# Performance work log

Hardware: AMD Instinct MI355X
Metric: run time of the kernel (lower is better)

The kernel has to match this reference:

```python
import jax, jax.numpy as jnp
import numpy as np
import math

ATTN_TEMP = 1.0


def bilinear_sample(fea, gx, gy):
    """fea: [B,C,Hs,Ws]; gx, gy: [B,N] pixel coords (align_corners=True), zero padding."""
    B, C, Hs, Ws = fea.shape
    x0 = jnp.floor(gx)
    y0 = jnp.floor(gy)
    x1 = x0 + 1.0
    y1 = y0 + 1.0
    wx1 = gx - x0
    wx0 = 1.0 - wx1
    wy1 = gy - y0
    wy0 = 1.0 - wy1
    flat = fea.reshape(B, C, Hs * Ws)

    def gather(xi, yi, w):
        valid = (xi >= 0) & (xi <= Ws - 1) & (yi >= 0) & (yi <= Hs - 1)
        xi_c = jnp.clip(xi, 0, Ws - 1).astype(jnp.int32)
        yi_c = jnp.clip(yi, 0, Hs - 1).astype(jnp.int32)
        idx = yi_c * Ws + xi_c  # [B,N]
        vals = jnp.take_along_axis(flat, idx[:, None, :], axis=2)  # [B,C,N]
        return vals * (w * valid.astype(fea.dtype))[:, None, :]

    return (gather(x0, y0, wx0 * wy0) + gather(x1, y0, wx1 * wy0)
            + gather(x0, y1, wx0 * wy1) + gather(x1, y1, wx1 * wy1))


def homo_warp(src_fea, src_proj, ref_proj, depth_values):
    """Plane-sweep homography warp. src_fea [B,C,Hs,Ws], projs [B,4,4], depth [B,D,Hr,Wr]."""
    B, C, Hs, Ws = src_fea.shape
    _, D, Hr, Wr = depth_values.shape
    proj = src_proj @ jnp.linalg.inv(ref_proj)
    rot = proj[:, :3, :3]
    trans = proj[:, :3, 3]  # [B,3]
    y, x = jnp.meshgrid(jnp.arange(Hr, dtype=src_fea.dtype),
                        jnp.arange(Wr, dtype=src_fea.dtype), indexing='ij')
    ones = jnp.ones(Hr * Wr, dtype=src_fea.dtype)
    xyz = jnp.stack([x.ravel(), y.ravel(), ones])  # [3,N]
    rot_xyz = jnp.einsum('bij,jn->bin', rot, xyz)  # [B,3,N]
    # [B,3,D,N]
    proj_xyz = rot_xyz[:, :, None, :] * depth_values.reshape(B, 1, D, Hr * Wr) \
               + trans[:, :, None, None]
    z = proj_xyz[:, 2]
    z = jnp.where(z == 0, jnp.asarray(1e-9, z.dtype), z)
    px = (proj_xyz[:, 0] / z).reshape(B, -1)  # pixel coords (equivalent to normalize+align_corners)
    py = (proj_xyz[:, 1] / z).reshape(B, -1)
    warped = bilinear_sample(src_fea, px, py)  # [B,C,D*Hr*Wr]
    return warped.reshape(B, C, D, Hr, Wr)


def make_proj(p):
    """p: [B,2,4,4] (extrinsic, intrinsic) -> combined [B,4,4]."""
    top = jnp.einsum('bij,bjk->bik', p[:, 1, :3, :3], p[:, 0, :3, :4])
    return p[:, 0].at[:, :3, :4].set(top)


def setup_inputs() -> dict:
    key = jax.random.key(0)
    k1, k2, k3 = jax.random.split(key, 3)
    V, B, C, H, W, D, G = 5, 2, 32, 128, 128, 32, 8
    features = jax.random.normal(k1, (V, B, C, H, W), dtype=jnp.float32)
    rng = np.random.default_rng(0)
    ext = np.tile(np.eye(4, dtype=np.float32), (B, V, 1, 1))
    ext[..., :3, :3] += 0.01 * rng.normal(size=(B, V, 3, 3)).astype(np.float32)
    ext[..., :3, 3] += 0.1 * rng.normal(size=(B, V, 3)).astype(np.float32)
    intr = np.tile(np.eye(4, dtype=np.float32), (B, V, 1, 1))
    intr[..., 0, 0] = 600.0
    intr[..., 1, 1] = 600.0
    intr[..., 0, 2] = W / 2.0
    intr[..., 1, 2] = H / 2.0
    proj_matrices = jnp.asarray(np.stack([ext, intr], axis=2))  # [B,V,2,4,4]
    base = jnp.linspace(425.0, 935.0, D, dtype=jnp.float32)[None, :, None, None]
    depth_hypo = base + 2.0 * jax.random.uniform(k2, (B, D, H, W), dtype=jnp.float32)
    reg_w = jax.random.normal(k3, (G,), dtype=jnp.float32)
    return {"features": features, "proj_matrices": proj_matrices,
            "depth_hypo": depth_hypo, "reg_w": reg_w}


def reference(features, proj_matrices, depth_hypo, reg_w):
    V = features.shape[0]
    ref_feature = features[0]
    B, C, H, W = ref_feature.shape
    D = depth_hypo.shape[1]
    G = reg_w.shape[0]
    ref_proj = make_proj(proj_matrices[:, 0])
    ref_vol = ref_feature.reshape(B, G, C // G, 1, H, W)
    dh_ng = jax.lax.stop_gradient(depth_hypo)  # warp grid is no_grad in torch
    cor_weight_sum = 1e-8
    cor_feats = 0.0
    inv_sqrt_c = 1.0 / math.sqrt(C)
    for v in range(1, V):
        src_proj = make_proj(proj_matrices[:, v])
        warped = homo_warp(features[v], jax.lax.stop_gradient(src_proj),
                           jax.lax.stop_gradient(ref_proj), dh_ng)
        # group correlation: [B,G,D,H,W]
        cor_feat = (warped.reshape(B, G, C // G, D, H, W) * ref_vol).mean(2)
        cor_weight = jax.nn.softmax(cor_feat.sum(1) / ATTN_TEMP, axis=1) * inv_sqrt_c
        cor_weight_sum = cor_weight_sum + cor_weight
        cor_feats = cor_feats + cor_weight[:, None] * cor_feat
    cor_feats = cor_feats / cor_weight_sum[:, None]
    logits = jnp.einsum('g,bgdhw->bdhw', reg_w, cor_feats)  # regnet stand-in
    attn_weight = jax.nn.softmax(logits, axis=1)
    idx = jnp.argmax(attn_weight, axis=1, keepdims=True)  # [B,1,H,W]
    depth = jnp.take_along_axis(depth_hypo, idx, axis=1)[:, 0]  # [B,H,W]
    return depth, attn_weight
```

## Files before the change

### kernel.cpp

```cpp
#include <hip/hip_runtime.h>
#include <math.h>

#pragma clang fp contract(off)

#define VV 5
#define BB 2
#define CC 32
#define HH 128
#define WW 128
#define DD 32
#define GG 8
#define HWW (HH*WW)
#define TRBLOCKS (VV*BB*(HWW/64))

typedef float v2f __attribute__((ext_vector_type(2)));

__global__ __launch_bounds__(256) void prep_kernel(const float* __restrict__ fea,
                                                   float* __restrict__ featT,
                                                   const float* __restrict__ pm,
                                                   float* __restrict__ wproj) {
#pragma clang fp contract(off)
    int t = threadIdx.x;
    if (blockIdx.x == TRBLOCKS) {
        int tid = t;
        if (tid >= BB * (VV - 1)) return;
        int b = tid / (VV - 1);
        int v = tid % (VV - 1) + 1;

        float refP[4][4], srcP[4][4];
        for (int which = 0; which < 2; which++) {
            int view = (which == 0) ? 0 : v;
            const float* base = pm + (size_t)(b * VV + view) * 2 * 16;
            const float* ext  = base;
            const float* intr = base + 16;
            float (*M)[4] = (which == 0) ? refP : srcP;
            for (int r = 0; r < 3; r++)
                for (int c = 0; c < 4; c++) {
                    float s = 0.f;
                    for (int k = 0; k < 3; k++)
                        s = fmaf(intr[r * 4 + k], ext[k * 4 + c], s);
                    M[r][c] = s;
                }
            for (int c = 0; c < 4; c++) M[3][c] = ext[12 + c];
        }

        float A[4][4];
        for (int r = 0; r < 4; r++)
            for (int c = 0; c < 4; c++) A[r][c] = refP[r][c];
        int ipiv[4];
        for (int j = 0; j < 4; j++) {
            int p = j; float amax = fabsf(A[j][j]);
            for (int i = j + 1; i < 4; i++) {
                float tt = fabsf(A[i][j]);
                if (tt > amax) { amax = tt; p = i; }
            }
            ipiv[j] = p;
            if (p != j)
                for (int c = 0; c < 4; c++) { float tt = A[j][c]; A[j][c] = A[p][c]; A[p][c] = tt; }
            float rcp = 1.0f / A[j][j];
            for (int i = j + 1; i < 4; i++) A[i][j] = A[i][j] * rcp;
            for (int i = j + 1; i < 4; i++)
                for (int k = j + 1; k < 4; k++)
                    A[i][k] = fmaf(-A[i][j], A[j][k], A[i][k]);
        }

        float Bm[4][4];
        for (int r = 0; r < 4; r++)
            for (int c = 0; c < 4; c++) Bm[r][c] = (r == c) ? 1.f : 0.f;
        for (int j = 0; j < 4; j++) {
            int p = ipiv[j];
            if (p != j)
                for (int c = 0; c < 4; c++) { float tt = Bm[j][c]; Bm[j][c] = Bm[p][c]; Bm[p][c] = tt; }
        }
        float invd[4];
        for (int k = 0; k < 4; k++) invd[k] = 1.0f / A[k][k];
        for (int c = 0; c < 4; c++) {
            for (int k = 0; k < 4; k++)
                for (int i = k + 1; i < 4; i++)
                    Bm[i][c] = fmaf(-A[i][k], Bm[k][c], Bm[i][c]);
            for (int k = 3; k >= 0; k--) {
                Bm[k][c] = Bm[k][c] * invd[k];
                for (int i = 0; i < k; i++)
                    Bm[i][c] = fmaf(-A[i][k], Bm[k][c], Bm[i][c]);
            }
        }

        float P[3][4];
        for (int r = 0; r < 3; r++)
            for (int c = 0; c < 4; c++) {
                float s = 0.f;
                for (int k = 0; k < 4; k++)
                    s = fmaf(srcP[r][k], Bm[k][c], s);
                P[r][c] = s;
            }
        float* o = wproj + (b * (VV - 1) + (v - 1)) * 12;
        for (int r = 0; r < 3; r++)
            for (int c = 0; c < 3; c++) o[r * 3 + c] = P[r][c];
        for (int r = 0; r < 3; r++) o[9 + r] = P[r][3];
        return;
    }

    __shared__ float tile[64][36];
    int vb = blockIdx.x >> 8;
    int base = (blockIdx.x & 255) * 64;
#pragma unroll
    for (int k = 0; k < 2; k++) {
        int c = (t >> 4) + 16 * k;
        int p = t & 15;
        float4 v = *(const float4*)&fea[((size_t)vb * CC + c) * HWW + base + 4 * p];
        int cs = c ^ ((p & 7) << 2);
        tile[4 * p + 0][cs] = v.x;
        tile[4 * p + 1][cs] = v.y;
        tile[4 * p + 2][cs] = v.z;
        tile[4 * p + 3][cs] = v.w;
    }
    __syncthreads();
#pragma unroll
    for (int m = 0; m < 2; m++) {
        int pl = (t >> 3) + 32 * m;
        int q = t & 7;
        int sw = ((pl >> 2) & 7) << 2;
        float4 v = *(const float4*)&tile[pl][(4 * q) ^ sw];
        *(float4*)&featT[((size_t)vb * HWW + base + pl) * CC + 4 * q] = v;
    }
}

__global__ __launch_bounds__(256) void main_kernel(const float* __restrict__ featT,
                                                   const float* __restrict__ wproj,
                                                   const float* __restrict__ depth_hypo,
                                                   const float* __restrict__ reg_w,
                                                   float* __restrict__ out) {
#pragma clang fp contract(off)
    __shared__ float s_ref[8][32];
    __shared__ float s_e[8][32];
    __shared__ float s_proj[4][12];
    __shared__ float s_regw[8];

    int t = threadIdx.x;
    int d = t & 31, pl = t >> 5;
    int base = t & 32;
    int pixbase = blockIdx.x * 8;
    int b = pixbase / HWW;
    int hwb = pixbase - b * HWW;

    s_ref[pl][d] = featT[((size_t)(b * HWW + hwb + pl)) * CC + d];
    if (t < 48) s_proj[t / 12][t % 12] = wproj[b * (VV - 1) * 12 + t];
    if (t < 8) s_regw[t] = reg_w[t];
    __syncthreads();

    int hw = hwb + pl;
    int y = hw >> 7, x = hw & (WW - 1);
    float fx = (float)x, fy = (float)y;
    float dep = depth_hypo[(size_t)(b * DD + d) * HWW + hw];

    float accs[8];
#pragma unroll
    for (int g = 0; g < 8; g++) accs[g] = 0.f;
    float cws = 1e-8f;

    for (int vi = 0; vi < 4; vi++) {
        const float* pr = s_proj[vi];
        float rx = fmaf(pr[1], fy, pr[0] * fx) + pr[2];
        float ry = fmaf(pr[4], fy, pr[3] * fx) + pr[5];
        float rz = fmaf(pr[7], fy, pr[6] * fx) + pr[8];
        float X = rx * dep + pr[9];
        float Y = ry * dep + pr[10];
        float Z = rz * dep + pr[11];
        if (Z == 0.f) Z = 1e-9f;
        float px = X / Z, py = Y / Z;

        float x0f = floorf(px), y0f = floorf(py);
        float x1f = x0f + 1.0f, y1f = y0f + 1.0f;
        float wx1 = px - x0f, wx0 = 1.0f - wx1;
        float wy1 = py - y0f, wy0 = 1.0f - wy1;
        bool vx0 = (x0f >= 0.f) && (x0f <= (float)(WW - 1));
        bool vx1 = (x1f >= 0.f) && (x1f <= (float)(WW - 1));
        bool vy0 = (y0f >= 0.f) && (y0f <= (float)(HH - 1));
        bool vy1 = (y1f >= 0.f) && (y1f <= (float)(HH - 1));

        int xc0 = (int)fminf(fmaxf(x0f, 0.f), (float)(WW - 1));
        int xc1 = (int)fminf(fmaxf(x1f, 0.f), (float)(WW - 1));
        int yc0 = (int)fminf(fmaxf(y0f, 0.f), (float)(HH - 1));
        int yc1 = (int)fminf(fmaxf(y1f, 0.f), (float)(HH - 1));

        float w00 = (wx0 * wy0) * ((vx0 && vy0) ? 1.f : 0.f);
        float w10 = (wx1 * wy0) * ((vx1 && vy0) ? 1.f : 0.f);
        float w01 = (wx0 * wy1) * ((vx0 && vy1) ? 1.f : 0.f);
        float w11 = (wx1 * wy1) * ((vx1 && vy1) ? 1.f : 0.f);

        v2f w00v = (v2f){w00, w00};
        v2f w10v = (v2f){w10, w10};
        v2f w01v = (v2f){w01, w01};
        v2f w11v = (v2f){w11, w11};

        const float* srcB = featT + (size_t)((vi + 1) * BB + b) * HWW * CC;
        const float* p00 = srcB + ((size_t)yc0 * WW + xc0) * CC;
        int dx = (xc1 - xc0) * CC;
        int dy = (yc1 - yc0) * (WW * CC);

        float cf[8];
        float s = 0.f;
#pragma unroll
        for (int g = 0; g < 8; g++) {
            float4 f00 = *(const float4*)(p00 + 4 * g);
            float4 f10 = *(const float4*)(p00 + dx + 4 * g);
            float4 f01 = *(const float4*)(p00 + dy + 4 * g);
            float4 f11 = *(const float4*)(p00 + dx + dy + 4 * g);
            v2f f00l = (v2f){f00.x, f00.y}, f00h = (v2f){f00.z, f00.w};
            v2f f10l = (v2f){f10.x, f10.y}, f10h = (v2f){f10.z, f10.w};
            v2f f01l = (v2f){f01.x, f01.y}, f01h = (v2f){f01.z, f01.w};
            v2f f11l = (v2f){f11.x, f11.y}, f11h = (v2f){f11.z, f11.w};

            v2f a = f00l * w00v;
            a = a + f10l * w10v;
            a = a + f01l * w01v;
            a = a + f11l * w11v;
            v2f bq = f00h * w00v;
            bq = bq + f10h * w10v;
            bq = bq + f01h * w01v;
            bq = bq + f11h * w11v;

            float4 r4 = *(const float4*)&s_ref[pl][g * 4];
            v2f refl = (v2f){r4.x, r4.y};
            v2f refh = (v2f){r4.z, r4.w};

            v2f prl = a * refl;
            v2f prh = bq * refh;

            float gs = prl.x;
            gs = gs + prl.y; gs = gs + prh.x; gs = gs + prh.y;
            gs = gs * 0.25f;
            cf[g] = gs;
            s = s + gs;
        }

        float m = s;
#pragma unroll
        for (int msk = 1; msk < 32; msk <<= 1) m = fmaxf(m, __shfl_xor(m, msk, 64));
        float e = expf(s - m);
        s_e[pl][d] = e;
        float sum = 0.f;
#pragma unroll
        for (int j = 0; j < 8; j++) {
            float4 q = *(const float4*)&s_e[pl][j * 4];
            sum = sum + q.x; sum = sum + q.y; sum = sum + q.z; sum = sum + q.w;
        }
        float cw = (e / sum) * 0.17677669529663687f;

        cws = cws + cw;
#pragma unroll
        for (int g = 0; g < 8; g++) {
            float tterm = cw * cf[g];
            accs[g] = accs[g] + tterm;
        }
    }

    float logit = 0.f;
#pragma unroll
    for (int g = 0; g < 8; g++) {
        float cfn = accs[g] / cws;
        logit = fmaf(s_regw[g], cfn, logit);
    }

    float m2 = logit;
#pragma unroll
    for (int msk = 1; msk < 32; msk <<= 1) m2 = fmaxf(m2, __shfl_xor(m2, msk, 64));
    float e2 = expf(logit - m2);
    s_e[pl][d] = e2;
    float s2 = 0.f;
#pragma unroll
    for (int j = 0; j < 8; j++) {
        float4 q = *(const float4*)&s_e[pl][j * 4];
        s2 = s2 + q.x; s2 = s2 + q.y; s2 = s2 + q.z; s2 = s2 + q.w;
    }
    float attn = e2 / s2;
    out[(size_t)BB * HWW + (size_t)(b * DD + d) * HWW + hw] = attn;

    float a1 = attn;
#pragma unroll
    for (int msk = 1; msk < 32; msk <<= 1) a1 = fmaxf(a1, __shfl_xor(a1, msk, 64));
    int idx1 = (attn == a1) ? d : 1000;
#pragma unroll
    for (int msk = 1; msk < 32; msk <<= 1) {
        int oi = __shfl_xor(idx1, msk, 64);
        idx1 = (oi < idx1) ? oi : idx1;
    }
    float dep1 = __shfl(dep, base + idx1, 64);
    if (d == 0) out[b * HWW + hw] = dep1;
}

extern "C" void kernel_launch(void* const* d_in, const int* in_sizes, int n_in,
                              void* d_out, int out_size, void* d_ws, size_t ws_size,
                              hipStream_t stream) {
    const float* features   = (const float*)d_in[0];
    const float* pm         = (const float*)d_in[1];
    const float* depth_hypo = (const float*)d_in[2];
    const float* reg_w      = (const float*)d_in[3];
    float* out = (float*)d_out;

    float* wproj = (float*)d_ws;
    float* featT = (float*)((char*)d_ws + 4096);

    prep_kernel<<<TRBLOCKS + 1, 256, 0, stream>>>(features, featT, pm, wproj);
    main_kernel<<<BB * HWW / 8, 256, 0, stream>>>(featT, wproj, depth_hypo, reg_w, out);
}
```

Measured before the change: 150.9 us.

## Parallelize source-view loop across threads with shared-memory reduction

The main kernel now launches 1024 threads per block, and each group of 256 threads handles one of the four source views in parallel instead of looping over views serially. Per-view correlation features and softmax weights are written to shared memory, then the first 256 threads combine them and run the final softmax and argmax. The aim is more memory-level parallelism for the gather loads and shorter per-thread dependency chains. The cost is more shared memory and a block-wide barrier, and three quarters of the threads sit idle during the tail.

New measurement: 156.3 us. +3.6%, slower.

```diff
diff --git a/kernel.cpp b/kernel.cpp
--- a/kernel.cpp
+++ b/kernel.cpp
@@ -125,132 +125,146 @@
     }
 }
 
-__global__ __launch_bounds__(256) void main_kernel(const float* __restrict__ featT,
-                                                   const float* __restrict__ wproj,
-                                                   const float* __restrict__ depth_hypo,
-                                                   const float* __restrict__ reg_w,
-                                                   float* __restrict__ out) {
+__global__ __launch_bounds__(1024) void main_kernel(const float* __restrict__ featT,
+                                                    const float* __restrict__ wproj,
+                                                    const float* __restrict__ depth_hypo,
+                                                    const float* __restrict__ reg_w,
+                                                    float* __restrict__ out) {
 #pragma clang fp contract(off)
     __shared__ float s_ref[8][32];
-    __shared__ float s_e[8][32];
+    __shared__ float s_e[32][32];
     __shared__ float s_proj[4][12];
     __shared__ float s_regw[8];
+    __shared__ float s_cw[8][4][32];
+    __shared__ float s_cf[8][4][8][32];
 
     int t = threadIdx.x;
-    int d = t & 31, pl = t >> 5;
+    int d   = t & 31;
+    int px  = (t >> 5) & 7;
+    int vi  = t >> 8;
+    int row = t >> 5;
     int base = t & 32;
+
     int pixbase = blockIdx.x * 8;
     int b = pixbase / HWW;
     int hwb = pixbase - b * HWW;
 
-    s_ref[pl][d] = featT[((size_t)(b * HWW + hwb + pl)) * CC + d];
+    if (t < 256) s_ref[row][d] = featT[((size_t)(b * HWW + hwb + row)) * CC + d];
     if (t < 48) s_proj[t / 12][t % 12] = wproj[b * (VV - 1) * 12 + t];
     if (t < 8) s_regw[t] = reg_w[t];
     __syncthreads();
 
-    int hw = hwb + pl;
+    int hw = hwb + px;
     int y = hw >> 7, x = hw & (WW - 1);
     float fx = (float)x, fy = (float)y;
     float dep = depth_hypo[(size_t)(b * DD + d) * HWW + hw];
 
+    const float* pr = s_proj[vi];
+    float rx = fmaf(pr[1], fy, pr[0] * fx) + pr[2];
+    float ry = fmaf(pr[4], fy, pr[3] * fx) + pr[5];
+    float rz = fmaf(pr[7], fy, pr[6] * fx) + pr[8];
+    float X = rx * dep + pr[9];
+    float Y = ry * dep + pr[10];
+    float Z = rz * dep + pr[11];
+    if (Z == 0.f) Z = 1e-9f;
+    float px_ = X / Z, py_ = Y / Z;
+
+    float x0f = floorf(px_), y0f = floorf(py_);
+    float x1f = x0f + 1.0f, y1f = y0f + 1.0f;
+    float wx1 = px_ - x0f, wx0 = 1.0f - wx1;
+    float wy1 = py_ - y0f, wy0 = 1.0f - wy1;
+    bool vx0 = (x0f >= 0.f) && (x0f <= (float)(WW - 1));
+    bool vx1 = (x1f >= 0.f) && (x1f <= (float)(WW - 1));
+    bool vy0 = (y0f >= 0.f) && (y0f <= (float)(HH - 1));
+    bool vy1 = (y1f >= 0.f) && (y1f <= (float)(HH - 1));
+
+    int xc0 = (int)fminf(fmaxf(x0f, 0.f), (float)(WW - 1));
+    int xc1 = (int)fminf(fmaxf(x1f, 0.f), (float)(WW - 1));
+    int yc0 = (int)fminf(fmaxf(y0f, 0.f), (float)(HH - 1));
+    int yc1 = (int)fminf(fmaxf(y1f, 0.f), (float)(HH - 1));
+
+    float w00 = (wx0 * wy0) * ((vx0 && vy0) ? 1.f : 0.f);
+    float w10 = (wx1 * wy0) * ((vx1 && vy0) ? 1.f : 0.f);
+    float w01 = (wx0 * wy1) * ((vx0 && vy1) ? 1.f : 0.f);
+    float w11 = (wx1 * wy1) * ((vx1 && vy1) ? 1.f : 0.f);
+
+    v2f w00v = (v2f){w00, w00};
+    v2f w10v = (v2f){w10, w10};
+    v2f w01v = (v2f){w01, w01};
+    v2f w11v = (v2f){w11, w11};
+
+    const float* srcB = featT + (size_t)((vi + 1) * BB + b) * HWW * CC;
+    const float* p00 = srcB + ((size_t)yc0 * WW + xc0) * CC;
+    int dx = (xc1 - xc0) * CC;
+    int dy = (yc1 - yc0) * (WW * CC);
+
+    float cf[8];
+    float s = 0.f;
+#pragma unroll
+    for (int g = 0; g < 8; g++) {
+        float4 f00 = *(const float4*)(p00 + 4 * g);
+        float4 f10 = *(const float4*)(p00 + dx + 4 * g);
+        float4 f01 = *(const float4*)(p00 + dy + 4 * g);
+        float4 f11 = *(const float4*)(p00 + dx + dy + 4 * g);
+        v2f f00l = (v2f){f00.x, f00.y}, f00h = (v2f){f00.z, f00.w};
+        v2f f10l = (v2f){f10.x, f10.y}, f10h = (v2f){f10.z, f10.w};
+        v2f f01l = (v2f){f01.x, f01.y}, f01h = (v2f){f01.z, f01.w};
+        v2f f11l = (v2f){f11.x, f11.y}, f11h = (v2f){f11.z, f11.w};
+
+        v2f a = f00l * w00v;
+        a = a + f10l * w10v;
+        a = a + f01l * w01v;
+        a = a + f11l * w11v;
+        v2f bq = f00h * w00v;
+        bq = bq + f10h * w10v;
+        bq = bq + f01h * w01v;
+        bq = bq + f11h * w11v;
+
+        float4 r4 = *(const float4*)&s_ref[px][g * 4];
+        v2f refl = (v2f){r4.x, r4.y};
+        v2f refh = (v2f){r4.z, r4.w};
+
+        v2f prl = a * refl;
+        v2f prh = bq * refh;
+
+        float gs = prl.x;
+        gs = gs + prl.y; gs = gs + prh.x; gs = gs + prh.y;
+        gs = gs * 0.25f;
+        cf[g] = gs;
+        s = s + gs;
+    }
+
+    float m = s;
+#pragma unroll
+    for (int msk = 1; msk < 32; msk <<= 1) m = fmaxf(m, __shfl_xor(m, msk, 64));
+    float e = expf(s - m);
+    s_e[row][d] = e;
+    float sum = 0.f;
+#pragma unroll
+    for (int j = 0; j < 8; j++) {
+        float4 q = *(const float4*)&s_e[row][j * 4];
+        sum = sum + q.x; sum = sum + q.y; sum = sum + q.z; sum = sum + q.w;
+    }
+    float cw = (e / sum) * 0.17677669529663687f;
+
+    s_cw[px][vi][d] = cw;
+#pragma unroll
+    for (int g = 0; g < 8; g++) s_cf[px][vi][g][d] = cf[g];
+    __syncthreads();
+
+    if (t >= 256) return;
+
+    float cws = 1e-8f;
     float accs[8];
 #pragma unroll
     for (int g = 0; g < 8; g++) accs[g] = 0.f;
-    float cws = 1e-8f;
-
-    for (int vi = 0; vi < 4; vi++) {
-        const float* pr = s_proj[vi];
-        float rx = fmaf(pr[1], fy, pr[0] * fx) + pr[2];
-        float ry = fmaf(pr[4], fy, pr[3] * fx) + pr[5];
-        float rz = fmaf(pr[7], fy, pr[6] * fx) + pr[8];
-        float X = rx * dep + pr[9];
-        float Y = ry * dep + pr[10];
-        float Z = rz * dep + pr[11];
-        if (Z == 0.f) Z = 1e-9f;
-        float px = X / Z, py = Y / Z;
-
-        float x0f = floorf(px), y0f = floorf(py);
-        float x1f = x0f + 1.0f, y1f = y0f + 1.0f;
-        float wx1 = px - x0f, wx0 = 1.0f - wx1;
-        float wy1 = py - y0f, wy0 = 1.0f - wy1;
-        bool vx0 = (x0f >= 0.f) && (x0f <= (float)(WW - 1));
-        bool vx1 = (x1f >= 0.f) && (x1f <= (float)(WW - 1));
-        bool vy0 = (y0f >= 0.f) && (y0f <= (float)(HH - 1));
-        bool vy1 = (y1f >= 0.f) && (y1f <= (float)(HH - 1));
-
-        int xc0 = (int)fminf(fmaxf(x0f, 0.f), (float)(WW - 1));
-        int xc1 = (int)fminf(fmaxf(x1f, 0.f), (float)(WW - 1));
-        int yc0 = (int)fminf(fmaxf(y0f, 0.f), (float)(HH - 1));
-        int yc1 = (int)fminf(fmaxf(y1f, 0.f), (float)(HH - 1));
-
-        float w00 = (wx0 * wy0) * ((vx0 && vy0) ? 1.f : 0.f);
-        float w10 = (wx1 * wy0) * ((vx1 && vy0) ? 1.f : 0.f);
-        float w01 = (wx0 * wy1) * ((vx0 && vy1) ? 1.f : 0.f);
-        float w11 = (wx1 * wy1) * ((vx1 && vy1) ? 1.f : 0.f);
-
-        v2f w00v = (v2f){w00, w00};
-        v2f w10v = (v2f){w10, w10};
-        v2f w01v = (v2f){w01, w01};
-        v2f w11v = (v2f){w11, w11};
-
-        const float* srcB = featT + (size_t)((vi + 1) * BB + b) * HWW * CC;
-        const float* p00 = srcB + ((size_t)yc0 * WW + xc0) * CC;
-        int dx = (xc1 - xc0) * CC;
-        int dy = (yc1 - yc0) * (WW * CC);
-
-        float cf[8];
-        float s = 0.f;
+#pragma unroll
+    for (int v = 0; v < 4; v++) {
+        float cwv = s_cw[px][v][d];
+        cws = cws + cwv;
 #pragma unroll
         for (int g = 0; g < 8; g++) {
-            float4 f00 = *(const float4*)(p00 + 4 * g);
-            float4 f10 = *(const float4*)(p00 + dx + 4 * g);
-            float4 f01 = *(const float4*)(p00 + dy + 4 * g);
-            float4 f11 = *(const float4*)(p00 + dx + dy + 4 * g);
-            v2f f00l = (v2f){f00.x, f00.y}, f00h = (v2f){f00.z, f00.w};
-            v2f f10l = (v2f){f10.x, f10.y}, f10h = (v2f){f10.z, f10.w};
-            v2f f01l = (v2f){f01.x, f01.y}, f01h = (v2f){f01.z, f01.w};
-            v2f f11l = (v2f){f11.x, f11.y}, f11h = (v2f){f11.z, f11.w};
-
-            v2f a = f00l * w00v;
-            a = a + f10l * w10v;
-            a = a + f01l * w01v;
-            a = a + f11l * w11v;
-            v2f bq = f00h * w00v;
-            bq = bq + f10h * w10v;
-            bq = bq + f01h * w01v;
-            bq = bq + f11h * w11v;
-
-            float4 r4 = *(const float4*)&s_ref[pl][g * 4];
-            v2f refl = (v2f){r4.x, r4.y};
-            v2f refh = (v2f){r4.z, r4.w};
-
-            v2f prl = a * refl;
-            v2f prh = bq * refh;
-
-            float gs = prl.x;
-            gs = gs + prl.y; gs = gs + prh.x; gs = gs + prh.y;
-            gs = gs * 0.25f;
-            cf[g] = gs;
-            s = s + gs;
-        }
-
-        float m = s;
-#pragma unroll
-        for (int msk = 1; msk < 32; msk <<= 1) m = fmaxf(m, __shfl_xor(m, msk, 64));
-        float e = expf(s - m);
-        s_e[pl][d] = e;
-        float sum = 0.f;
-#pragma unroll
-        for (int j = 0; j < 8; j++) {
-            float4 q = *(const float4*)&s_e[pl][j * 4];
-            sum = sum + q.x; sum = sum + q.y; sum = sum + q.z; sum = sum + q.w;
-        }
-        float cw = (e / sum) * 0.17677669529663687f;
-
-        cws = cws + cw;
-#pragma unroll
-        for (int g = 0; g < 8; g++) {
-            float tterm = cw * cf[g];
+            float tterm = cwv * s_cf[px][v][g][d];
             accs[g] = accs[g] + tterm;
         }
     }
@@ -266,11 +280,11 @@
 #pragma unroll
     for (int msk = 1; msk < 32; msk <<= 1) m2 = fmaxf(m2, __shfl_xor(m2, msk, 64));
     float e2 = expf(logit - m2);
-    s_e[pl][d] = e2;
+    s_e[px][d] = e2;
     float s2 = 0.f;
 #pragma unroll
     for (int j = 0; j < 8; j++) {
-        float4 q = *(const float4*)&s_e[pl][j * 4];
+        float4 q = *(const float4*)&s_e[px][j * 4];
         s2 = s2 + q.x; s2 = s2 + q.y; s2 = s2 + q.z; s2 = s2 + q.w;
     }
     float attn = e2 / s2;
@@ -302,5 +316,5 @@
     float* featT = (float*)((char*)d_ws + 4096);
 
     prep_kernel<<<TRBLOCKS + 1, 256, 0, stream>>>(features, featT, pm, wproj);
-    main_kernel<<<BB * HWW / 8, 256, 0, stream>>>(featT, wproj, depth_hypo, reg_w, out);
+    main_kernel<<<BB * HWW / 8, 1024, 0, stream>>>(featT, wproj, depth_hypo, reg_w, out);
 }
```
